# Kernel tuning notes

Hardware: AMD Instinct MI355X
Metric: run time of the kernel (lower is better)

## Reference

```python
import jax, jax.numpy as jnp
import numpy as np

N, M, K, D = 65536, 131072, 8, 64
TAU = 0.3
EPS = 1e-6

def setup_inputs() -> dict:
    key = jax.random.key(0)
    ks = jax.random.split(key, 16)
    s = 0.05
    return {
        "f_pts": jax.random.normal(ks[0], (N, D), jnp.float32),
        "pts": jax.random.uniform(ks[1], (N, 3), jnp.float32) * 10.0,
        "z_latent": jax.random.normal(ks[2], (M, D), jnp.float32) * 0.1,
        "centers": jax.random.uniform(ks[3], (M, 3), jnp.float32) * 10.0,
        "cand_idx": jax.random.randint(ks[4], (N, K), 0, M),
        "sim_w1": jax.random.normal(ks[5], (2 * D + 3, 64), jnp.float32) * s,
        "sim_b1": jnp.zeros((64,), jnp.float32),
        "sim_w2": jax.random.normal(ks[6], (64, 1), jnp.float32) * s,
        "sim_b2": jnp.zeros((1,), jnp.float32),
        "gate_w1": jax.random.normal(ks[7], (2 * D, D), jnp.float32) * s,
        "gate_b1": jnp.zeros((D,), jnp.float32),
        "gate_w2": jax.random.normal(ks[8], (D, 1), jnp.float32) * s,
        "gate_b2": jnp.zeros((1,), jnp.float32),
        "W_ih": jax.random.normal(ks[9], (3 * D, D), jnp.float32) * s,
        "W_hh": jax.random.normal(ks[10], (3 * D, D), jnp.float32) * s,
        "b_ih": jnp.zeros((3 * D,), jnp.float32),
        "b_hh": jnp.zeros((3 * D,), jnp.float32),
    }

def _forward(f_pts, pts, z_latent, centers, sim_w1, sim_b1, sim_w2, sim_b2,
             gate_w1, gate_b1, gate_w2, gate_b2, W_ih, W_hh, b_ih, b_hh, cand_idx):
    n, k = cand_idx.shape
    m, d = z_latent.shape
    # --- gather voxel latents / centers for each (point, candidate) pair ---
    z_c = z_latent[cand_idx]                         # (N,K,D)
    delta = pts[:, None, :] - centers[cand_idx]      # (N,K,3)
    f_b = jnp.broadcast_to(f_pts[:, None, :], (n, k, d))
    # --- similarity MLP ---
    x = jnp.concatenate([f_b, z_c, delta], axis=-1)  # (N,K,2D+3)
    h = jax.nn.relu(x @ sim_w1 + sim_b1)
    sim = (h @ sim_w2 + sim_b2)[..., 0]              # (N,K)
    # --- low-temperature top-K routing weights over candidates ---
    w = jax.nn.softmax(sim / TAU, axis=-1)           # (N,K)
    # --- scatter weighted point features to voxels ---
    flat_idx = cand_idx.reshape(-1)                  # (N*K,)
    contrib = (w[..., None] * f_pts[:, None, :]).reshape(-1, d)
    msg = jax.ops.segment_sum(contrib, flat_idx, num_segments=m)     # (M,D)
    wsum = jax.ops.segment_sum(w.reshape(-1), flat_idx, num_segments=m)
    msg = msg / (wsum[:, None] + EPS)                # normalized voxel message
    # --- per-voxel gate ---
    g_in = jnp.concatenate([z_latent, msg], axis=-1)
    gate = jax.nn.sigmoid(jax.nn.relu(g_in @ gate_w1 + gate_b1) @ gate_w2 + gate_b2)  # (M,1)
    # --- GRUCell (torch layout: rows ordered r,z,n) ---
    gi = msg @ W_ih.T + b_ih
    gh = z_latent @ W_hh.T + b_hh
    i_r, i_z, i_n = jnp.split(gi, 3, axis=-1)
    h_r, h_z, h_n = jnp.split(gh, 3, axis=-1)
    r = jax.nn.sigmoid(i_r + h_r)
    zg = jax.nn.sigmoid(i_z + h_z)
    nn_ = jnp.tanh(i_n + r * h_n)
    h_new = (1.0 - zg) * nn_ + zg * z_latent
    # gated latent update
    return z_latent + gate * (h_new - z_latent)

def reference(f_pts, pts, z_latent, centers, cand_idx, sim_w1, sim_b1, sim_w2, sim_b2,
              gate_w1, gate_b1, gate_w2, gate_b2, W_ih, W_hh, b_ih, b_hh):
    return _forward(f_pts, pts, z_latent, centers, sim_w1, sim_b1, sim_w2, sim_b2,
                    gate_w1, gate_b1, gate_w2, gate_b2, W_ih, W_hh, b_ih, b_hh, cand_idx)
```

## Files before the change

kernel.cpp:

```cpp
#include <hip/hip_runtime.h>
#include <hip/hip_fp16.h>
#include <math.h>


typedef short bf16x8 __attribute__((ext_vector_type(8)));
typedef unsigned short u16x8 __attribute__((ext_vector_type(8)));
typedef float f32x4 __attribute__((ext_vector_type(4)));
#define MFMA __builtin_amdgcn_mfma_f32_16x16x32_bf16
#define CAP 32

__device__ __forceinline__ short f2bf(float f) {
  unsigned u = __float_as_uint(f);
  unsigned r = (u + 0x7FFFu + ((u >> 16) & 1u)) >> 16;
  return (short)r;
}

__device__ __forceinline__ float bf2f(unsigned short h) {
  return __uint_as_float(((unsigned)h) << 16);
}

__device__ __forceinline__ float sigm(float x) { return 1.0f / (1.0f + __expf(-x)); }

__global__ __launch_bounds__(256) void zero_cursor(int* __restrict__ c, int m) {
  int n4 = m >> 2;
  int stride = gridDim.x * 256;
  int4* p = (int4*)c;
  for (int j = blockIdx.x * 256 + threadIdx.x; j < n4; j += stride)
    p[j] = make_int4(0, 0, 0, 0);
}

__global__ __launch_bounds__(256) void prep_kernel(
    const float* __restrict__ z, const float* __restrict__ f,
    const float* __restrict__ sim_w1, const float* __restrict__ sim_b1,
    const float* __restrict__ gate_w1, const float* __restrict__ W_ih,
    const float* __restrict__ W_hh, const int* __restrict__ cand,
    unsigned short* __restrict__ zbf, unsigned short* __restrict__ fbf,
    unsigned short* __restrict__ HBt, short* __restrict__ bfZ,
    short* __restrict__ GF, short* __restrict__ WihF, short* __restrict__ WhhF,
    int* __restrict__ slotbuf, int* __restrict__ cursor, int M, long npairs)
{
  long tid = (long)blockIdx.x * 256 + threadIdx.x;
  long nthr = (long)gridDim.x * 256;

  for (long i = tid; i < npairs; i += nthr)
    slotbuf[i] = atomicAdd(&cursor[cand[i]], 1);

  long nz = (long)M * 64;
  for (long i = tid * 8; i < nz; i += nthr * 8) {
    float4 a = *(const float4*)&z[i];
    float4 b4 = *(const float4*)&z[i + 4];
    u16x8 o;
    o[0] = (unsigned short)f2bf(a.x);  o[1] = (unsigned short)f2bf(a.y);
    o[2] = (unsigned short)f2bf(a.z);  o[3] = (unsigned short)f2bf(a.w);
    o[4] = (unsigned short)f2bf(b4.x); o[5] = (unsigned short)f2bf(b4.y);
    o[6] = (unsigned short)f2bf(b4.z); o[7] = (unsigned short)f2bf(b4.w);
    *(u16x8*)&zbf[i] = o;
  }

  if (blockIdx.x == gridDim.x - 1 && threadIdx.x < 64) {
    int lane = threadIdx.x;
    int lr = lane & 15, lg = lane >> 4;
#pragma unroll
    for (int ct = 0; ct < 4; ++ct)
#pragma unroll
      for (int kt = 0; kt < 3; ++kt) {
        bf16x8 b;
#pragma unroll
        for (int e = 0; e < 8; ++e) {
          int k = kt * 32 + lg * 8 + e;
          float v = (k < 67) ? sim_w1[(64 + k) * 64 + ct * 16 + lr] : 0.0f;
          b[e] = f2bf(v);
        }
        *(bf16x8*)&bfZ[(ct * 3 + kt) * 512 + lane * 8] = b;
      }
  }

  if (blockIdx.x >= 1024 && blockIdx.x < 1040) {
    int fb = (blockIdx.x - 1024) * 4 + (threadIdx.x >> 6);
    int lane = threadIdx.x & 63, lr = lane & 15, lg = lane >> 4;
    bf16x8 o;
    if (fb < 16) {
      int ct = fb >> 2, kt = fb & 3;
#pragma unroll
      for (int e = 0; e < 8; ++e)
        o[e] = f2bf(gate_w1[(kt * 32 + lg * 8 + e) * 64 + ct * 16 + lr]);
      *(bf16x8*)&GF[fb * 512 + lane * 8] = o;
    } else if (fb < 40) {
      int q = fb - 16, g = q >> 3, ct = (q >> 1) & 3, k2 = q & 1;
      int row = g * 64 + ct * 16 + lr;
#pragma unroll
      for (int e = 0; e < 8; ++e)
        o[e] = f2bf(W_ih[row * 64 + k2 * 32 + lg * 8 + e]);
      *(bf16x8*)&WihF[q * 512 + lane * 8] = o;
    } else {
      int q = fb - 40, g = q >> 3, ct = (q >> 1) & 3, k2 = q & 1;
      int row = g * 64 + ct * 16 + lr;
#pragma unroll
      for (int e = 0; e < 8; ++e)
        o[e] = f2bf(W_hh[row * 64 + k2 * 32 + lg * 8 + e]);
      *(bf16x8*)&WhhF[q * 512 + lane * 8] = o;
    }
  }

  if (blockIdx.x < 1024) {
    int wave = blockIdx.x * 4 + (threadIdx.x >> 6);
    int lane = threadIdx.x & 63;
    int lr = lane & 15, lg = lane >> 4;
    int n0 = wave * 16;

    bf16x8 bf[8];
#pragma unroll
    for (int ct = 0; ct < 4; ++ct)
#pragma unroll
      for (int kt = 0; kt < 2; ++kt) {
        bf16x8 bb;
#pragma unroll
        for (int e = 0; e < 8; ++e)
          bb[e] = f2bf(sim_w1[(kt * 32 + lg * 8 + e) * 64 + ct * 16 + lr]);
        bf[ct * 2 + kt] = bb;
      }

    bf16x8 a[2];
#pragma unroll
    for (int kt = 0; kt < 2; ++kt) {
      const float* src = &f[(long)(n0 + lr) * 64 + kt * 32 + lg * 8];
      float4 v0 = *(const float4*)src;
      float4 v1 = *(const float4*)(src + 4);
      bf16x8 t;
      t[0] = f2bf(v0.x); t[1] = f2bf(v0.y); t[2] = f2bf(v0.z); t[3] = f2bf(v0.w);
      t[4] = f2bf(v1.x); t[5] = f2bf(v1.y); t[6] = f2bf(v1.z); t[7] = f2bf(v1.w);
      a[kt] = t;
    }
    *(bf16x8*)&fbf[(long)(n0 + lr) * 64 + lg * 8] = a[0];
    *(bf16x8*)&fbf[(long)(n0 + lr) * 64 + 32 + lg * 8] = a[1];

    f32x4 acc[4] = {{0,0,0,0},{0,0,0,0},{0,0,0,0},{0,0,0,0}};
#pragma unroll
    for (int ct = 0; ct < 4; ++ct) {
      acc[ct] = MFMA(a[0], bf[ct * 2 + 0], acc[ct], 0, 0, 0);
      acc[ct] = MFMA(a[1], bf[ct * 2 + 1], acc[ct], 0, 0, 0);
    }
    float b10 = sim_b1[lr], b11 = sim_b1[16 + lr];
    float b12 = sim_b1[32 + lr], b13 = sim_b1[48 + lr];
#pragma unroll
    for (int e = 0; e < 4; ++e) {
      unsigned lo = (unsigned)(unsigned short)f2bf(acc[0][e] + b10)
                  | ((unsigned)(unsigned short)f2bf(acc[1][e] + b11) << 16);
      unsigned hi = (unsigned)(unsigned short)f2bf(acc[2][e] + b12)
                  | ((unsigned)(unsigned short)f2bf(acc[3][e] + b13) << 16);
      *(uint2*)&HBt[(long)(n0 + lg * 4 + e) * 64 + lr * 4] = make_uint2(lo, hi);
    }
  }
}

#define TPW 4
__global__ __launch_bounds__(256) void pair_kernel(
    const float* __restrict__ pts, const unsigned short* __restrict__ zbf,
    const float* __restrict__ centers, const int* __restrict__ cand_idx,
    const float* __restrict__ sim_w2, const short* __restrict__ bfZ,
    const unsigned short* __restrict__ HBt,
    const int* __restrict__ slotbuf, unsigned* __restrict__ rec)
{
  int wave = (blockIdx.x * 256 + threadIdx.x) >> 6;
  int lane = threadIdx.x & 63;
  int lr = lane & 15, lg = lane >> 4;

  int call = cand_idx[wave * 64 + lane];
  int slot = slotbuf[wave * 64 + lane];

  bf16x8 b[12];
#pragma unroll
  for (int i = 0; i < 12; ++i) b[i] = *(const bf16x8*)&bfZ[i * 512 + lane * 8];
  float w2c[4];
#pragma unroll
  for (int ct = 0; ct < 4; ++ct) w2c[ct] = sim_w2[ct * 16 + lr];

  int c[TPW];
  bf16x8 a0[TPW], a1[TPW], ad[TPW];
  uint2 h2[TPW];
#pragma unroll
  for (int t = 0; t < TPW; ++t) {
    c[t] = __shfl(call, t * 16 + lr, 64);
    a0[t] = *(const bf16x8*)&zbf[(long)c[t] * 64 + lg * 8];
    a1[t] = *(const bf16x8*)&zbf[(long)c[t] * 64 + 32 + lg * 8];
    h2[t] = *(const uint2*)&HBt[((long)(wave * TPW + t) * 2 + (lg >> 1)) * 64 + lr * 4];
    bf16x8 tt = {0, 0, 0, 0, 0, 0, 0, 0};
    if (lg == 0) {
      int n = (wave * TPW + t) * 2 + (lr >> 3);
      tt[0] = f2bf(pts[n * 3 + 0] - centers[c[t] * 3 + 0]);
      tt[1] = f2bf(pts[n * 3 + 1] - centers[c[t] * 3 + 1]);
      tt[2] = f2bf(pts[n * 3 + 2] - centers[c[t] * 3 + 2]);
    }
    ad[t] = tt;
  }

  f32x4 part[TPW];
#pragma unroll
  for (int t = 0; t < TPW; ++t) {
    f32x4 acc[4] = {{0,0,0,0},{0,0,0,0},{0,0,0,0},{0,0,0,0}};
#pragma unroll
    for (int ct = 0; ct < 4; ++ct) {
      acc[ct] = MFMA(a0[t], b[ct * 3 + 0], acc[ct], 0, 0, 0);
      acc[ct] = MFMA(a1[t], b[ct * 3 + 1], acc[ct], 0, 0, 0);
      acc[ct] = MFMA(ad[t], b[ct * 3 + 2], acc[ct], 0, 0, 0);
    }
    float hb[4];
    hb[0] = bf2f((unsigned short)(h2[t].x));
    hb[1] = bf2f((unsigned short)(h2[t].x >> 16));
    hb[2] = bf2f((unsigned short)(h2[t].y));
    hb[3] = bf2f((unsigned short)(h2[t].y >> 16));
    f32x4 p = {0.f, 0.f, 0.f, 0.f};
#pragma unroll
    for (int ct = 0; ct < 4; ++ct)
#pragma unroll
      for (int e = 0; e < 4; ++e)
        p[e] = fmaf(fmaxf(acc[ct][e] + hb[ct], 0.0f), w2c[ct], p[e]);
    part[t] = p;
  }

  float wrow[TPW];
#pragma unroll
  for (int t = 0; t < TPW; ++t) {
    f32x4 p = part[t];
#pragma unroll
    for (int m = 1; m <= 8; m <<= 1)
#pragma unroll
      for (int e = 0; e < 4; ++e) p[e] += __shfl_xor(p[e], m, 64);
    float other[4];
#pragma unroll
    for (int e = 0; e < 4; ++e) other[e] = __shfl_xor(p[e], 16, 64);
    float mx = p[0];
#pragma unroll
    for (int e = 1; e < 4; ++e) mx = fmaxf(mx, p[e]);
#pragma unroll
    for (int e = 0; e < 4; ++e) mx = fmaxf(mx, other[e]);
    float ex[4], se = 0.f, so = 0.f;
#pragma unroll
    for (int e = 0; e < 4; ++e) {
      ex[e] = __expf((p[e] - mx) * (1.0f / 0.3f));
      se += ex[e];
      so += __expf((other[e] - mx) * (1.0f / 0.3f));
    }
    float inv = 1.0f / (se + so);
    int srcl = (lane >> 2) << 4;
    float t0 = __shfl(ex[0] * inv, srcl, 64);
    float t1 = __shfl(ex[1] * inv, srcl, 64);
    float t2 = __shfl(ex[2] * inv, srcl, 64);
    float t3 = __shfl(ex[3] * inv, srcl, 64);
    int esel = lane & 3;
    wrow[t] = esel == 0 ? t0 : esel == 1 ? t1 : esel == 2 ? t2 : t3;
  }

  float v0 = __shfl(wrow[0], lr, 64);
  float v1 = __shfl(wrow[1], lr, 64);
  float v2 = __shfl(wrow[2], lr, 64);
  float v3 = __shfl(wrow[3], lr, 64);
  float wv = lg == 0 ? v0 : lg == 1 ? v1 : lg == 2 ? v2 : v3;

  if (slot < CAP) {
    int n_pt = wave * 8 + 2 * lg + (lr >> 3);
    unsigned short wh = __half_as_ushort(__float2half(wv));
    rec[(long)call * CAP + slot] = ((unsigned)n_pt << 16) | (unsigned)wh;
  }
}

__global__ __launch_bounds__(256) void gather_kernel(
    const unsigned* __restrict__ rec, const int* __restrict__ cursor,
    const unsigned short* __restrict__ fbf, unsigned short* __restrict__ msg_bf,
    int mvox)
{
  int tid = blockIdx.x * 256 + threadIdx.x;
  int row = tid >> 2, seg = tid & 3;
  if (row >= mvox) return;

  int cnt = cursor[row];
  cnt = cnt < CAP ? cnt : CAP;
  const unsigned* rp = &rec[(long)row * CAP];

  float acc[16];
#pragma unroll
  for (int j = 0; j < 16; ++j) acc[j] = 0.f;
  float ws = 0.f;

  for (int i0 = 0; i0 < cnt; i0 += 4) {
    uint4 r4 = *(const uint4*)&rp[i0];
    unsigned rr0 = r4.x, rr1 = r4.y, rr2 = r4.z, rr3 = r4.w;
#pragma unroll
    for (int j = 0; j < 4; ++j) {
      unsigned r = j == 0 ? rr0 : j == 1 ? rr1 : j == 2 ? rr2 : rr3;
      if (i0 + j < cnt) {
        float w = __half2float(__ushort_as_half((unsigned short)(r & 0xffffu)));
        int n = r >> 16;
        ws += w;
        const u16x8* fp = (const u16x8*)&fbf[(long)n * 64 + seg * 16];
        u16x8 f0 = fp[0], f1 = fp[1];
#pragma unroll
        for (int k = 0; k < 8; ++k) {
          acc[k]     = fmaf(w, bf2f(f0[k]), acc[k]);
          acc[8 + k] = fmaf(w, bf2f(f1[k]), acc[8 + k]);
        }
      }
    }
  }
  float inv = 1.0f / (ws + 1e-6f);
  u16x8 o0, o1;
#pragma unroll
  for (int j = 0; j < 8; ++j) {
    o0[j] = (unsigned short)f2bf(acc[j] * inv);
    o1[j] = (unsigned short)f2bf(acc[8 + j] * inv);
  }
  *(u16x8*)&msg_bf[(long)row * 64 + seg * 16] = o0;
  *(u16x8*)&msg_bf[(long)row * 64 + seg * 16 + 8] = o1;
}

__global__ __launch_bounds__(512)
__attribute__((amdgpu_waves_per_eu(2)))
void stage2(
    const unsigned short* __restrict__ zbf,
    const short* __restrict__ GF, const short* __restrict__ WihF,
    const short* __restrict__ WhhF,
    const float* __restrict__ gate_b1, const float* __restrict__ gate_w2,
    const float* __restrict__ gate_b2,
    const float* __restrict__ b_ih, const float* __restrict__ b_hh,
    const unsigned short* __restrict__ msg_bf,
    float* __restrict__ out)
{
  __shared__ float gb1s[64], gw2s[64], bihs[192], bhhs[192];
  __shared__ float gb2s;

  int t = threadIdx.x;
  if (t < 64) { gb1s[t] = gate_b1[t]; gw2s[t] = gate_w2[t]; }
  if (t < 192) { bihs[t] = b_ih[t]; bhhs[t] = b_hh[t]; }
  if (t == 0) gb2s = gate_b2[0];
  __syncthreads();

  int wid = t >> 6, lane = t & 63;
  int lr = lane & 15, lg = lane >> 4;

  int rowbase = blockIdx.x * 128 + wid * 16;
  long abase = (long)(rowbase + lr) * 64;
  bf16x8 a0 = *(const bf16x8*)&zbf[abase + lg * 8];
  bf16x8 a1 = *(const bf16x8*)&zbf[abase + 32 + lg * 8];
  bf16x8 a2 = *(const bf16x8*)&msg_bf[abase + lg * 8];
  bf16x8 a3 = *(const bf16x8*)&msg_bf[abase + 32 + lg * 8];

  f32x4 usum = {0.f, 0.f, 0.f, 0.f};
#pragma unroll 1
  for (int ct = 0; ct < 4; ++ct) {
    f32x4 au = {0, 0, 0, 0};
    au = MFMA(a0, *(const bf16x8*)&GF[(ct * 4 + 0) * 512 + lane * 8], au, 0, 0, 0);
    au = MFMA(a1, *(const bf16x8*)&GF[(ct * 4 + 1) * 512 + lane * 8], au, 0, 0, 0);
    au = MFMA(a2, *(const bf16x8*)&GF[(ct * 4 + 2) * 512 + lane * 8], au, 0, 0, 0);
    au = MFMA(a3, *(const bf16x8*)&GF[(ct * 4 + 3) * 512 + lane * 8], au, 0, 0, 0);
    int c = ct * 16 + lr;
#pragma unroll
    for (int e = 0; e < 4; ++e)
      usum[e] += fmaxf(au[e] + gb1s[c], 0.0f) * gw2s[c];
  }
#pragma unroll
  for (int m = 1; m <= 8; m <<= 1)
#pragma unroll
    for (int e = 0; e < 4; ++e) {
      float v = usum[e];
      usum[e] = v + __shfl_xor(v, m, 64);
    }
  float gate[4];
#pragma unroll
  for (int e = 0; e < 4; ++e) gate[e] = sigm(usum[e] + gb2s);

#pragma unroll 1
  for (int ct = 0; ct < 4; ++ct) {
    f32x4 air = {0,0,0,0}, aiz = {0,0,0,0}, ain = {0,0,0,0};
    f32x4 ahr = {0,0,0,0}, ahz = {0,0,0,0}, ahn = {0,0,0,0};
#pragma unroll
    for (int k2 = 0; k2 < 2; ++k2) {
      bf16x8 amg = k2 ? a3 : a2;
      bf16x8 az_ = k2 ? a1 : a0;
      int base = ct * 2 + k2;
      air = MFMA(amg, *(const bf16x8*)&WihF[(      base) * 512 + lane * 8], air, 0, 0, 0);
      aiz = MFMA(amg, *(const bf16x8*)&WihF[( 8 +  base) * 512 + lane * 8], aiz, 0, 0, 0);
      ain = MFMA(amg, *(const bf16x8*)&WihF[(16 +  base) * 512 + lane * 8], ain, 0, 0, 0);
      ahr = MFMA(az_, *(const bf16x8*)&WhhF[(      base) * 512 + lane * 8], ahr, 0, 0, 0);
      ahz = MFMA(az_, *(const bf16x8*)&WhhF[( 8 +  base) * 512 + lane * 8], ahz, 0, 0, 0);
      ahn = MFMA(az_, *(const bf16x8*)&WhhF[(16 +  base) * 512 + lane * 8], ahn, 0, 0, 0);
    }
    int c = ct * 16 + lr;
#pragma unroll
    for (int e = 0; e < 4; ++e) {
      float zv = bf2f(zbf[(long)(rowbase + lg * 4 + e) * 64 + c]);
      float rr = sigm(air[e] + bihs[c] + ahr[e] + bhhs[c]);
      float zg = sigm(aiz[e] + bihs[64 + c] + ahz[e] + bhhs[64 + c]);
      float nn = tanhf(ain[e] + bihs[128 + c] + rr * (ahn[e] + bhhs[128 + c]));
      float hnew = (1.0f - zg) * nn + zg * zv;
      out[(long)(rowbase + lg * 4 + e) * 64 + c] = zv + gate[e] * (hnew - zv);
    }
  }
}

extern "C" void kernel_launch(void* const* d_in, const int* in_sizes, int n_in,
                              void* d_out, int out_size, void* d_ws, size_t ws_size,
                              hipStream_t stream) {
  const float* f_pts   = (const float*)d_in[0];
  const float* pts     = (const float*)d_in[1];
  const float* z_lat   = (const float*)d_in[2];
  const float* centers = (const float*)d_in[3];
  const int*   cand    = (const int*)d_in[4];
  const float* sim_w1  = (const float*)d_in[5];
  const float* sim_b1  = (const float*)d_in[6];
  const float* sim_w2  = (const float*)d_in[7];
  const float* gate_w1 = (const float*)d_in[9];
  const float* gate_b1 = (const float*)d_in[10];
  const float* gate_w2 = (const float*)d_in[11];
  const float* gate_b2 = (const float*)d_in[12];
  const float* W_ih    = (const float*)d_in[13];
  const float* W_hh    = (const float*)d_in[14];
  const float* b_ih    = (const float*)d_in[15];
  const float* b_hh    = (const float*)d_in[16];

  int N = in_sizes[0] / 64;
  int M = in_sizes[2] / 64;

  int* cursor = (int*)d_ws;
  unsigned* rec = (unsigned*)(cursor + M);
  unsigned short* msg_bf = (unsigned short*)rec;
  unsigned short* zbf = (unsigned short*)(rec + (size_t)M * CAP);
  unsigned short* fbf = zbf + (size_t)M * 64;
  unsigned short* HBt = fbf + (size_t)N * 64;
  short* bfZ = (short*)(HBt + (size_t)N * 64);
  short* GF = bfZ + 12 * 512;
  short* WihF = GF + 16 * 512;
  short* WhhF = WihF + 24 * 512;
  int* slotbuf = (int*)(WhhF + 24 * 512);

  long npairs = (long)N * 8;

  zero_cursor<<<128, 256, 0, stream>>>(cursor, M);

  prep_kernel<<<2048, 256, 0, stream>>>(z_lat, f_pts, sim_w1, sim_b1,
                                        gate_w1, W_ih, W_hh, cand,
                                        zbf, fbf, HBt, bfZ, GF, WihF, WhhF,
                                        slotbuf, cursor, M, npairs);

  int nwaves = (N * 8) / (16 * TPW);
  pair_kernel<<<nwaves / 4, 256, 0, stream>>>(pts, zbf, centers, cand,
                                              sim_w2, bfZ, HBt, slotbuf, rec);

  gather_kernel<<<(M * 4) / 256, 256, 0, stream>>>(rec, cursor, fbf, msg_bf, M);

  stage2<<<M / 128, 512, 0, stream>>>(zbf, GF, WihF, WhhF,
                                      gate_b1, gate_w2, gate_b2, b_ih, b_hh,
                                      msg_bf, (float*)d_out);
}
```

Measured before the change: 115.6 us.

## Move slot atomics into pair kernel and fold cursor zeroing into prep

Removes the separate zero_cursor launch and instead zeroes the per-voxel cursor inside prep_kernel. Drops the slotbuf pass in prep_kernel, which took atomics over all pairs and wrote the results to memory; pair_kernel now takes the atomicAdd slot itself right before writing its record. This saves one kernel launch, one global write and one read of slotbuf, and lets the atomic latency overlap with pair compute. The sim_w1 projection work is spread across even waves of all 2048 blocks rather than the first 1024 blocks. Slot order becomes nondeterministic, which only matters when a voxel overflows CAP.

```diff
diff --git a/kernel.cpp b/kernel.cpp
--- a/kernel.cpp
+++ b/kernel.cpp
@@ -21,29 +21,20 @@
 
 __device__ __forceinline__ float sigm(float x) { return 1.0f / (1.0f + __expf(-x)); }
 
-__global__ __launch_bounds__(256) void zero_cursor(int* __restrict__ c, int m) {
-  int n4 = m >> 2;
-  int stride = gridDim.x * 256;
-  int4* p = (int4*)c;
-  for (int j = blockIdx.x * 256 + threadIdx.x; j < n4; j += stride)
-    p[j] = make_int4(0, 0, 0, 0);
-}
-
 __global__ __launch_bounds__(256) void prep_kernel(
     const float* __restrict__ z, const float* __restrict__ f,
     const float* __restrict__ sim_w1, const float* __restrict__ sim_b1,
     const float* __restrict__ gate_w1, const float* __restrict__ W_ih,
-    const float* __restrict__ W_hh, const int* __restrict__ cand,
+    const float* __restrict__ W_hh,
     unsigned short* __restrict__ zbf, unsigned short* __restrict__ fbf,
     unsigned short* __restrict__ HBt, short* __restrict__ bfZ,
     short* __restrict__ GF, short* __restrict__ WihF, short* __restrict__ WhhF,
-    int* __restrict__ slotbuf, int* __restrict__ cursor, int M, long npairs)
+    int* __restrict__ cursor, int M)
 {
   long tid = (long)blockIdx.x * 256 + threadIdx.x;
   long nthr = (long)gridDim.x * 256;
 
-  for (long i = tid; i < npairs; i += nthr)
-    slotbuf[i] = atomicAdd(&cursor[cand[i]], 1);
+  for (long i = tid; i < M; i += nthr) cursor[i] = 0;
 
   long nz = (long)M * 64;
   for (long i = tid * 8; i < nz; i += nthr * 8) {
@@ -102,53 +93,56 @@
     }
   }
 
-  if (blockIdx.x < 1024) {
-    int wave = blockIdx.x * 4 + (threadIdx.x >> 6);
-    int lane = threadIdx.x & 63;
-    int lr = lane & 15, lg = lane >> 4;
-    int n0 = wave * 16;
-
-    bf16x8 bf[8];
-#pragma unroll
-    for (int ct = 0; ct < 4; ++ct)
+  {
+    int g = blockIdx.x * 4 + (threadIdx.x >> 6);
+    if ((g & 1) == 0) {
+      int wave = g >> 1;
+      int lane = threadIdx.x & 63;
+      int lr = lane & 15, lg = lane >> 4;
+      int n0 = wave * 16;
+
+      bf16x8 bf[8];
+#pragma unroll
+      for (int ct = 0; ct < 4; ++ct)
+#pragma unroll
+        for (int kt = 0; kt < 2; ++kt) {
+          bf16x8 bb;
+#pragma unroll
+          for (int e = 0; e < 8; ++e)
+            bb[e] = f2bf(sim_w1[(kt * 32 + lg * 8 + e) * 64 + ct * 16 + lr]);
+          bf[ct * 2 + kt] = bb;
+        }
+
+      bf16x8 a[2];
 #pragma unroll
       for (int kt = 0; kt < 2; ++kt) {
-        bf16x8 bb;
-#pragma unroll
-        for (int e = 0; e < 8; ++e)
-          bb[e] = f2bf(sim_w1[(kt * 32 + lg * 8 + e) * 64 + ct * 16 + lr]);
-        bf[ct * 2 + kt] = bb;
+        const float* src = &f[(long)(n0 + lr) * 64 + kt * 32 + lg * 8];
+        float4 v0 = *(const float4*)src;
+        float4 v1 = *(const float4*)(src + 4);
+        bf16x8 t;
+        t[0] = f2bf(v0.x); t[1] = f2bf(v0.y); t[2] = f2bf(v0.z); t[3] = f2bf(v0.w);
+        t[4] = f2bf(v1.x); t[5] = f2bf(v1.y); t[6] = f2bf(v1.z); t[7] = f2bf(v1.w);
+        a[kt] = t;
       }
-
-    bf16x8 a[2];
-#pragma unroll
-    for (int kt = 0; kt < 2; ++kt) {
-      const float* src = &f[(long)(n0 + lr) * 64 + kt * 32 + lg * 8];
-      float4 v0 = *(const float4*)src;
-      float4 v1 = *(const float4*)(src + 4);
-      bf16x8 t;
-      t[0] = f2bf(v0.x); t[1] = f2bf(v0.y); t[2] = f2bf(v0.z); t[3] = f2bf(v0.w);
-      t[4] = f2bf(v1.x); t[5] = f2bf(v1.y); t[6] = f2bf(v1.z); t[7] = f2bf(v1.w);
-      a[kt] = t;
-    }
-    *(bf16x8*)&fbf[(long)(n0 + lr) * 64 + lg * 8] = a[0];
-    *(bf16x8*)&fbf[(long)(n0 + lr) * 64 + 32 + lg * 8] = a[1];
-
-    f32x4 acc[4] = {{0,0,0,0},{0,0,0,0},{0,0,0,0},{0,0,0,0}};
-#pragma unroll
-    for (int ct = 0; ct < 4; ++ct) {
-      acc[ct] = MFMA(a[0], bf[ct * 2 + 0], acc[ct], 0, 0, 0);
-      acc[ct] = MFMA(a[1], bf[ct * 2 + 1], acc[ct], 0, 0, 0);
-    }
-    float b10 = sim_b1[lr], b11 = sim_b1[16 + lr];
-    float b12 = sim_b1[32 + lr], b13 = sim_b1[48 + lr];
-#pragma unroll
-    for (int e = 0; e < 4; ++e) {
-      unsigned lo = (unsigned)(unsigned short)f2bf(acc[0][e] + b10)
-                  | ((unsigned)(unsigned short)f2bf(acc[1][e] + b11) << 16);
-      unsigned hi = (unsigned)(unsigned short)f2bf(acc[2][e] + b12)
-                  | ((unsigned)(unsigned short)f2bf(acc[3][e] + b13) << 16);
-      *(uint2*)&HBt[(long)(n0 + lg * 4 + e) * 64 + lr * 4] = make_uint2(lo, hi);
+      *(bf16x8*)&fbf[(long)(n0 + lr) * 64 + lg * 8] = a[0];
+      *(bf16x8*)&fbf[(long)(n0 + lr) * 64 + 32 + lg * 8] = a[1];
+
+      f32x4 acc[4] = {{0,0,0,0},{0,0,0,0},{0,0,0,0},{0,0,0,0}};
+#pragma unroll
+      for (int ct = 0; ct < 4; ++ct) {
+        acc[ct] = MFMA(a[0], bf[ct * 2 + 0], acc[ct], 0, 0, 0);
+        acc[ct] = MFMA(a[1], bf[ct * 2 + 1], acc[ct], 0, 0, 0);
+      }
+      float b10 = sim_b1[lr], b11 = sim_b1[16 + lr];
+      float b12 = sim_b1[32 + lr], b13 = sim_b1[48 + lr];
+#pragma unroll
+      for (int e = 0; e < 4; ++e) {
+        unsigned lo = (unsigned)(unsigned short)f2bf(acc[0][e] + b10)
+                    | ((unsigned)(unsigned short)f2bf(acc[1][e] + b11) << 16);
+        unsigned hi = (unsigned)(unsigned short)f2bf(acc[2][e] + b12)
+                    | ((unsigned)(unsigned short)f2bf(acc[3][e] + b13) << 16);
+        *(uint2*)&HBt[(long)(n0 + lg * 4 + e) * 64 + lr * 4] = make_uint2(lo, hi);
+      }
     }
   }
 }
@@ -159,14 +153,13 @@
     const float* __restrict__ centers, const int* __restrict__ cand_idx,
     const float* __restrict__ sim_w2, const short* __restrict__ bfZ,
     const unsigned short* __restrict__ HBt,
-    const int* __restrict__ slotbuf, unsigned* __restrict__ rec)
+    int* __restrict__ cursor, unsigned* __restrict__ rec)
 {
   int wave = (blockIdx.x * 256 + threadIdx.x) >> 6;
   int lane = threadIdx.x & 63;
   int lr = lane & 15, lg = lane >> 4;
 
   int call = cand_idx[wave * 64 + lane];
-  int slot = slotbuf[wave * 64 + lane];
 
   bf16x8 b[12];
 #pragma unroll
@@ -250,6 +243,8 @@
     int esel = lane & 3;
     wrow[t] = esel == 0 ? t0 : esel == 1 ? t1 : esel == 2 ? t2 : t3;
   }
+
+  int slot = atomicAdd(&cursor[call], 1);
 
   float v0 = __shfl(wrow[0], lr, 64);
   float v1 = __shfl(wrow[1], lr, 64);
@@ -430,20 +425,15 @@
   short* GF = bfZ + 12 * 512;
   short* WihF = GF + 16 * 512;
   short* WhhF = WihF + 24 * 512;
-  int* slotbuf = (int*)(WhhF + 24 * 512);
-
-  long npairs = (long)N * 8;
-
-  zero_cursor<<<128, 256, 0, stream>>>(cursor, M);
 
   prep_kernel<<<2048, 256, 0, stream>>>(z_lat, f_pts, sim_w1, sim_b1,
-                                        gate_w1, W_ih, W_hh, cand,
+                                        gate_w1, W_ih, W_hh,
                                         zbf, fbf, HBt, bfZ, GF, WihF, WhhF,
-                                        slotbuf, cursor, M, npairs);
+                                        cursor, M);
 
   int nwaves = (N * 8) / (16 * TPW);
   pair_kernel<<<nwaves / 4, 256, 0, stream>>>(pts, zbf, centers, cand,
-                                              sim_w2, bfZ, HBt, slotbuf, rec);
+                                              sim_w2, bfZ, HBt, cursor, rec);
 
   gather_kernel<<<(M * 4) / 256, 256, 0, stream>>>(rec, cursor, fbf, msg_bf, M);
 
```

Measured after the change: 108.6 us. 1.06x faster.
